# Optimization experiments

Measured on AMD Instinct MI355X. Metric: run time of the kernel, lower is better.

The kernel has to match this reference:

```python
import jax, jax.numpy as jnp
import numpy as np

B, N, C, H = 8, 16384, 256, 128
FG_NPOINT = 4096
SAMPLE_POINT = 1024
MAX_TRANSLATE = jnp.array([3.0, 3.0, 2.0], dtype=jnp.float32)


def _fps(xyz, n_sample):
    # xyz: [N,3] -> indices [n_sample] (D-FPS, seed index 0)
    d0 = jnp.sum((xyz - xyz[0]) ** 2, axis=-1)  # [N]

    def body(dists, _):
        idx = jnp.argmax(dists)
        d = jnp.sum((xyz - xyz[idx]) ** 2, axis=-1)
        return jnp.minimum(dists, d), idx

    _, idxs = jax.lax.scan(body, d0, None, length=n_sample - 1)
    return jnp.concatenate([jnp.zeros((1,), dtype=idxs.dtype), idxs])


def fps_batch(xyz, n_sample):
    return jax.vmap(lambda p: _fps(p, n_sample))(xyz)  # [B, n_sample]


def gather_pts(xyz, idx):
    # xyz [B,N,3], idx [B,S] -> [B,S,3]
    return jnp.take_along_axis(xyz, idx[..., None], axis=1)


def gather_feat(feat, idx):
    # feat [B,C,N], idx [B,S] -> [B,C,S]
    return jnp.take_along_axis(feat, idx[:, None, :], axis=2)


def setup_inputs() -> dict:
    key = jax.random.key(0)
    ks = jax.random.split(key, 6)
    return {
        "xyz": jax.random.normal(ks[0], (B, N, 3), jnp.float32) * 10.0,
        "features": jax.random.normal(ks[1], (B, C, N), jnp.float32),
        "seg_w1": jax.random.normal(ks[2], (H, C), jnp.float32) * 0.05,
        "seg_scale1": jnp.ones((H,), jnp.float32),
        "seg_bias1": jnp.zeros((H,), jnp.float32),
        "seg_w2": jax.random.normal(ks[3], (1, H), jnp.float32) * 0.05,
        "seg_b2": jnp.zeros((1,), jnp.float32),
        "vote_w1": jax.random.normal(ks[4], (H, C), jnp.float32) * 0.05,
        "vote_scale1": jnp.ones((H,), jnp.float32),
        "vote_bias1": jnp.zeros((H,), jnp.float32),
        "reg_w": jax.random.normal(ks[5], (3, H), jnp.float32) * 0.05,
        "reg_b": jnp.zeros((3,), jnp.float32),
    }


def reference(xyz, features, seg_w1, seg_scale1, seg_bias1, seg_w2, seg_b2,
              vote_w1, vote_scale1, vote_bias1, reg_w, reg_b):
    # ---- seg branch: 1x1 conv + BN(eval affine) + ReLU, then 1x1 conv to num_class
    h = jax.nn.relu(jnp.einsum('oc,bcn->bon', seg_w1, features)
                    * seg_scale1[None, :, None] + seg_bias1[None, :, None])
    seg = jnp.einsum('oc,bon->bcn'.replace('c', 'k'), seg_w2, h)  # [B,1,N]
    seg = seg + seg_b2[None, :, None]
    seg_score = jax.nn.sigmoid(jnp.max(seg, axis=1))  # [B,N] (max over class dim)

    # ---- top-k foreground selection
    _, fg_idx = jax.lax.top_k(seg_score, FG_NPOINT)  # [B,M]
    fg_xyz = gather_pts(xyz, fg_idx)                  # [B,M,3]
    fg_feat = gather_feat(features, fg_idx)           # [B,C,M]

    # ---- vote/offset layer (3DSSD-style): MLP -> clamped offset
    vh = jax.nn.relu(jnp.einsum('oc,bcm->bom', vote_w1, fg_feat)
                     * vote_scale1[None, :, None] + vote_bias1[None, :, None])  # [B,H,M]
    reg = jnp.einsum('oh,bhm->bom', reg_w, vh) + reg_b[None, :, None]  # [B,3,M]
    offset = jnp.clip(reg.transpose(0, 2, 1), -MAX_TRANSLATE, MAX_TRANSLATE)  # [B,M,3]
    fg_xyz_ctr = fg_xyz + offset
    fg_feat_ctr = vh

    # ---- original-point FPS sampler + gathers
    ori_idx = fps_batch(fg_xyz, SAMPLE_POINT)
    sampled_ori_xyz = gather_pts(fg_xyz, ori_idx)
    sampled_ori_feat = gather_feat(fg_feat, ori_idx)

    # ---- center-point FPS sampler + gathers
    ctr_idx = fps_batch(fg_xyz_ctr, SAMPLE_POINT)
    sampled_ctr_xyz = gather_pts(fg_xyz_ctr, ctr_idx)
    sampled_ctr_feat = gather_feat(fg_feat_ctr, ctr_idx)
    sampled_ctr_offset = gather_pts(offset, ctr_idx)
    sampled_ctr_origin = gather_pts(fg_xyz, ctr_idx)

    # ---- aggregation concat (USE_ORIGINAL_POINT=True)
    agg_xyz = jnp.concatenate([sampled_ctr_xyz, sampled_ori_xyz], axis=1)       # [B,2S,3]
    agg_feat = jnp.concatenate([sampled_ctr_feat, sampled_ori_feat[:, :H, :]], axis=-1)  # [B,H,2S]

    return (agg_xyz, agg_feat, sampled_ctr_xyz, sampled_ctr_offset,
            sampled_ctr_origin, seg)
```

## Files before the change

### kernel.cpp

```cpp
#include <hip/hip_runtime.h>

#define NB 8
#define NP 16384
#define NC 256
#define NH 128
#define NM 4096
#define NS 1024

typedef float v2f __attribute__((ext_vector_type(2)));

__device__ __forceinline__ unsigned long long make_key(float v, int n) {
  unsigned u = __float_as_uint(v);
  u = (u & 0x80000000u) ? ~u : (u | 0x80000000u);
  unsigned d = ~u;
  return (((unsigned long long)d) << 32) | (unsigned)n;
}

__device__ __forceinline__ float wave_max_dpp(float v) {
#define DPPMAX(ctrl)                                                            \
  v = fmaxf(v, __int_as_float(__builtin_amdgcn_update_dpp(                      \
                 __float_as_int(v), __float_as_int(v), (ctrl), 0xf, 0xf, false)))
  DPPMAX(0xB1);
  DPPMAX(0x4E);
  DPPMAX(0x141);
  DPPMAX(0x140);
  DPPMAX(0x142);
  DPPMAX(0x143);
#undef DPPMAX
  return __int_as_float(__builtin_amdgcn_readlane(__float_as_int(v), 63));
}

__global__ __launch_bounds__(256) void transpose_w_kernel(
    const float* __restrict__ wseg, const float* __restrict__ wvote,
    float* __restrict__ tseg, float* __restrict__ tvote) {
  int i = blockIdx.x * 256 + threadIdx.x;
  int c = i >> 7, o = i & 127;
  tseg[i] = wseg[o * NC + c];
  tvote[i] = wvote[o * NC + c];
}

__global__ __launch_bounds__(256) void seg_kernel(
    const float* __restrict__ features, const float* __restrict__ w1t,
    const float* __restrict__ scale1, const float* __restrict__ bias1,
    const float* __restrict__ w2, const float* __restrict__ b2,
    float* __restrict__ seg_out, unsigned long long* __restrict__ keys) {
  __shared__ float wt[32][128];
  __shared__ float ft[32][128];
  __shared__ float red[16][128];
  __shared__ float Ssh[128];
  __shared__ float w2sh[128];
  int b = blockIdx.y;
  int n0 = blockIdx.x * 128;
  int tid = threadIdx.x;
  int lane = tid & 63;
  int ro = tid >> 4, rc = tid & 15;
  float a0 = w2[lane], a1 = w2[lane + 64];
  float whi = fmaxf(a0, a1), wlo = fminf(a0, a1);
#pragma unroll
  for (int off = 32; off >= 1; off >>= 1) {
    whi = fmaxf(whi, __shfl_xor(whi, off, 64));
    wlo = fminf(wlo, __shfl_xor(wlo, off, 64));
  }
  if (tid < 128) w2sh[tid] = w2[tid];
  const float* fb = features + (size_t)b * NC * NP;
  float acc[8][8] = {};
  for (int kc = 0; kc < NC; kc += 32) {
#pragma unroll
    for (int t = 0; t < 4; ++t) {
      int q = tid + t * 256;
      int kk = q >> 5, c4 = (q & 31) * 4;
      *(float4*)&wt[kk][c4] = *(const float4*)&w1t[(kc + kk) * NH + c4];
    }
#pragma unroll
    for (int t = 0; t < 4; ++t) {
      int q = tid + t * 256;
      int kk = q >> 5, c4 = (q & 31) * 4;
      *(float4*)&ft[kk][c4] = *(const float4*)&fb[(size_t)(kc + kk) * NP + n0 + c4];
    }
    __syncthreads();
#pragma unroll
    for (int kk = 0; kk < 32; ++kk) {
      float wv[8], fv[8];
#pragma unroll
      for (int i = 0; i < 8; ++i) wv[i] = wt[kk][ro * 8 + i];
#pragma unroll
      for (int j = 0; j < 8; ++j) fv[j] = ft[kk][rc * 8 + j];
#pragma unroll
      for (int i = 0; i < 8; ++i)
#pragma unroll
        for (int j = 0; j < 8; ++j) acc[i][j] = fmaf(wv[i], fv[j], acc[i][j]);
    }
    __syncthreads();
  }
  float part[8] = {};
#pragma unroll
  for (int i = 0; i < 8; ++i) {
    int o = ro * 8 + i;
    float sc = scale1[o], bi = bias1[o];
#pragma unroll
    for (int j = 0; j < 8; ++j) {
      float h = fmaxf(fmaf(acc[i][j], sc, bi), 0.0f);
      part[j] += h;
    }
  }
#pragma unroll
  for (int j = 0; j < 8; ++j) red[ro][rc * 8 + j] = part[j];
  __syncthreads();
  float b2v = b2[0];
  if (tid < 128) {
    float S = 0.0f;
#pragma unroll
    for (int r = 0; r < 16; ++r) S += red[r][tid];
    Ssh[tid] = S;
    float m = (S >= 0.0f ? whi * S : wlo * S) + b2v;
    float sig = 1.0f / (1.0f + expf(-m));
    int nn = n0 + tid;
    keys[(size_t)b * NP + nn] = make_key(sig, nn);
  }
  __syncthreads();
#pragma unroll
  for (int t = 0; t < 16; ++t) {
    int q = tid + t * 256;
    int k = q >> 5, n4 = (q & 31) * 4;
    float w2k = w2sh[k];
    const float4 s4 = *(const float4*)&Ssh[n4];
    float4 sv;
    sv.x = fmaf(w2k, s4.x, b2v);
    sv.y = fmaf(w2k, s4.y, b2v);
    sv.z = fmaf(w2k, s4.z, b2v);
    sv.w = fmaf(w2k, s4.w, b2v);
    *(float4*)&seg_out[((size_t)b * 128 + k) * NP + n0 + n4] = sv;
  }
}

__global__ __launch_bounds__(1024) void sort8k_kernel(unsigned long long* __restrict__ keys) {
  __shared__ unsigned long long sk[8192];
  int chunk = blockIdx.x & 1, b = blockIdx.x >> 1;
  bool desc = (chunk == 1);
  unsigned long long* K = keys + (size_t)b * NP + chunk * 8192;
  int tid = threadIdx.x;
  for (int i = tid; i < 8192; i += 1024) sk[i] = K[i];
  __syncthreads();
  for (int k = 2; k <= 8192; k <<= 1) {
    for (int j = k >> 1; j > 0; j >>= 1) {
      for (int i = tid; i < 8192; i += 1024) {
        int ixj = i ^ j;
        if (ixj > i) {
          bool up = (((i & k) == 0) != desc);
          unsigned long long a = sk[i], c = sk[ixj];
          if ((a > c) == up) { sk[i] = c; sk[ixj] = a; }
        }
      }
      __syncthreads();
    }
  }
  for (int i = tid; i < 8192; i += 1024) K[i] = sk[i];
}

__global__ __launch_bounds__(1024) void merge_topk_kernel(
    const unsigned long long* __restrict__ keys, int* __restrict__ fg_idx,
    float* __restrict__ fg_xyz, const float* __restrict__ xyz) {
  __shared__ unsigned long long sk[8192];
  int b = blockIdx.x;
  const unsigned long long* K = keys + (size_t)b * NP;
  int tid = threadIdx.x;
  for (int i = tid; i < 8192; i += 1024) {
    unsigned long long a = K[i], c = K[i + 8192];
    sk[i] = (a < c) ? a : c;
  }
  __syncthreads();
  for (int j = 4096; j > 0; j >>= 1) {
    for (int i = tid; i < 8192; i += 1024) {
      int ixj = i ^ j;
      if (ixj > i) {
        unsigned long long a = sk[i], c = sk[ixj];
        if (a > c) { sk[i] = c; sk[ixj] = a; }
      }
    }
    __syncthreads();
  }
  for (int m = tid; m < NM; m += 1024) {
    unsigned long long key = sk[m];
    int idx = (int)(key & 0xffffffffULL);
    fg_idx[b * NM + m] = idx;
    size_t src = ((size_t)b * NP + idx) * 3;
    size_t dst = ((size_t)b * NM + m) * 3;
    fg_xyz[dst + 0] = xyz[src + 0];
    fg_xyz[dst + 1] = xyz[src + 1];
    fg_xyz[dst + 2] = xyz[src + 2];
  }
}

__global__ __launch_bounds__(256) void vote_kernel(
    const float* __restrict__ features, const int* __restrict__ fg_idx,
    const float* __restrict__ w1t, const float* __restrict__ scale1,
    const float* __restrict__ bias1, const float* __restrict__ rw,
    const float* __restrict__ rb, const float* __restrict__ fg_xyz,
    float* __restrict__ vh, float* __restrict__ offs, float* __restrict__ fg_ctr) {
  __shared__ float wt[32][128];
  __shared__ float ft[32][64];
  __shared__ float hl[128][65];
  __shared__ int idx_l[64];
  int b = blockIdx.y;
  int m0 = blockIdx.x * 64;
  int tid = threadIdx.x;
  int ro = tid >> 4, rc = tid & 15;
  const float* fb = features + (size_t)b * NC * NP;
  if (tid < 64) idx_l[tid] = fg_idx[b * NM + m0 + tid];
  __syncthreads();
  float acc[8][4] = {};
  for (int kc = 0; kc < NC; kc += 32) {
    for (int q = tid; q < 4096; q += 256) {
      int kk = q >> 7, o = q & 127;
      wt[kk][o] = w1t[(kc + kk) * NH + o];
    }
    for (int q = tid; q < 2048; q += 256) {
      int kk = q >> 6, mm = q & 63;
      ft[kk][mm] = fb[(size_t)(kc + kk) * NP + idx_l[mm]];
    }
    __syncthreads();
#pragma unroll
    for (int kk = 0; kk < 32; ++kk) {
      float wv[8], fv[4];
#pragma unroll
      for (int i = 0; i < 8; ++i) wv[i] = wt[kk][ro * 8 + i];
#pragma unroll
      for (int j = 0; j < 4; ++j) fv[j] = ft[kk][rc * 4 + j];
#pragma unroll
      for (int i = 0; i < 8; ++i)
#pragma unroll
        for (int j = 0; j < 4; ++j) acc[i][j] = fmaf(wv[i], fv[j], acc[i][j]);
    }
    __syncthreads();
  }
#pragma unroll
  for (int i = 0; i < 8; ++i) {
    int o = ro * 8 + i;
    float sc = scale1[o], bi = bias1[o];
#pragma unroll
    for (int j = 0; j < 4; ++j) {
      float h = fmaxf(fmaf(acc[i][j], sc, bi), 0.0f);
      hl[o][rc * 4 + j] = h;
      vh[((size_t)b * NH + o) * NM + m0 + rc * 4 + j] = h;
    }
  }
  __syncthreads();
  if (tid < 64) {
    int m = m0 + tid;
    const float MT[3] = {3.0f, 3.0f, 2.0f};
#pragma unroll
    for (int r = 0; r < 3; ++r) {
      float a = 0.0f;
      for (int o = 0; o < NH; ++o) a = fmaf(rw[r * NH + o], hl[o][tid], a);
      a += rb[r];
      a = fminf(fmaxf(a, -MT[r]), MT[r]);
      size_t p = ((size_t)b * NM + m) * 3 + r;
      offs[p] = a;
      fg_ctr[p] = __fadd_rn(fg_xyz[p], a);
    }
  }
}

#define PPT 16
__global__ __launch_bounds__(256) void fps_kernel(
    const float* __restrict__ fg_xyz, const float* __restrict__ fg_ctr,
    int* __restrict__ ori_idx, int* __restrict__ ctr_idx) {
#pragma clang fp contract(off)
  __shared__ float px[NM], py[NM], pz[NM];
  __shared__ __align__(32) unsigned long long wkey[2][4];
  __shared__ int sel_list[NS];
  int set = blockIdx.x & 1, b = blockIdx.x >> 1;
  const float* P = (set == 0 ? fg_xyz : fg_ctr) + (size_t)b * NM * 3;
  int* O = (set == 0 ? ori_idx : ctr_idx) + b * NS;
  int tid = threadIdx.x;
  for (int m = tid; m < NM; m += 256) {
    px[m] = P[m * 3 + 0];
    py[m] = P[m * 3 + 1];
    pz[m] = P[m * 3 + 2];
  }
  __syncthreads();
  v2f x2[8], y2[8], z2[8], d2[8];
  int base_idx = tid * PPT;
#pragma unroll
  for (int j = 0; j < 8; ++j) {
    int m0 = base_idx + 2 * j, m1 = m0 + 1;
    v2f t;
    t.x = px[m0]; t.y = px[m1]; x2[j] = t;
    t.x = py[m0]; t.y = py[m1]; y2[j] = t;
    t.x = pz[m0]; t.y = pz[m1]; z2[j] = t;
    t.x = 3.402823466e38f; t.y = 3.402823466e38f;
    d2[j] = t;
  }
  if (tid == 0) sel_list[0] = 0;
  int lane = tid & 63, wave = tid >> 6;
  float sx = px[0], sy = py[0], sz = pz[0];
  for (int it = 1; it < NS; ++it) {
    v2f sxv, syv, szv;
    sxv.x = sx; sxv.y = sx;
    syv.x = sy; syv.y = sy;
    szv.x = sz; szv.y = sz;
    float bd = -1.0f;
    int bc = base_idx;
#pragma unroll
    for (int j = 0; j < 8; ++j) {
      v2f dx = x2[j] - sxv, dy = y2[j] - syv, dz = z2[j] - szv;
      v2f dd = (dx * dx + dy * dy) + dz * dz;
      v2f nd;
      nd.x = fminf(d2[j].x, dd.x);
      nd.y = fminf(d2[j].y, dd.y);
      d2[j] = nd;
      if (j == 0) {
        bd = nd.x; bc = base_idx;
        bool g = nd.y > bd; bd = g ? nd.y : bd; bc = g ? base_idx + 1 : bc;
      } else {
        bool g0 = nd.x > bd; bd = g0 ? nd.x : bd; bc = g0 ? base_idx + 2 * j : bc;
        bool g1 = nd.y > bd; bd = g1 ? nd.y : bd; bc = g1 ? base_idx + 2 * j + 1 : bc;
      }
    }
    float wm = wave_max_dpp(bd);
    unsigned long long msk = __ballot(bd == wm);
    int wl = __ffsll((long long)msk) - 1;
    if (lane == wl)
      wkey[it & 1][wave] =
          (((unsigned long long)__float_as_uint(bd)) << 32) | (unsigned)(4095 - bc);
    __syncthreads();
    const ulonglong2* wk = (const ulonglong2*)&wkey[it & 1][0];
    ulonglong2 q0 = wk[0], q1 = wk[1];
    unsigned long long m0 = q0.x > q0.y ? q0.x : q0.y;
    unsigned long long m1 = q1.x > q1.y ? q1.x : q1.y;
    unsigned long long km = m0 > m1 ? m0 : m1;
    int sel = 4095 - (int)(km & 0xffffffffULL);
    if (tid == 0) sel_list[it] = sel;
    sx = px[sel]; sy = py[sel]; sz = pz[sel];
  }
  __syncthreads();
  for (int s2 = tid; s2 < NS; s2 += 256) O[s2] = sel_list[s2];
}

__global__ __launch_bounds__(256) void feat_out_kernel(
    const float* __restrict__ vh, const float* __restrict__ features,
    const int* __restrict__ fg_idx, const int* __restrict__ ori_idx,
    const int* __restrict__ ctr_idx, float* __restrict__ out_feat) {
  int b = blockIdx.z;
  int o = blockIdx.y * 4 + (threadIdx.x >> 6);
  int s = blockIdx.x * 64 + (threadIdx.x & 63);
  float val;
  if (s < NS) {
    int i = ctr_idx[b * NS + s];
    val = vh[((size_t)b * NH + o) * NM + i];
  } else {
    int i = ori_idx[b * NS + (s - NS)];
    int g = fg_idx[b * NM + i];
    val = features[((size_t)b * NC + o) * NP + g];
  }
  out_feat[((size_t)b * NH + o) * (2 * NS) + s] = val;
}

__global__ __launch_bounds__(256) void xyz_out_kernel(
    const float* __restrict__ fg_xyz, const float* __restrict__ fg_ctr,
    const float* __restrict__ offs, const int* __restrict__ ori_idx,
    const int* __restrict__ ctr_idx, float* __restrict__ out_agg,
    float* __restrict__ out_cxyz, float* __restrict__ out_coff,
    float* __restrict__ out_corg) {
  int b = blockIdx.y;
  int s = blockIdx.x * 256 + threadIdx.x;
  if (s < NS) {
    int i = ctr_idx[b * NS + s];
    size_t src = ((size_t)b * NM + i) * 3;
    size_t d_agg = ((size_t)b * 2 * NS + s) * 3;
    size_t d_s = ((size_t)b * NS + s) * 3;
#pragma unroll
    for (int r = 0; r < 3; ++r) {
      float c = fg_ctr[src + r];
      out_agg[d_agg + r] = c;
      out_cxyz[d_s + r] = c;
      out_coff[d_s + r] = offs[src + r];
      out_corg[d_s + r] = fg_xyz[src + r];
    }
  } else {
    int i = ori_idx[b * NS + (s - NS)];
    size_t src = ((size_t)b * NM + i) * 3;
    size_t d_agg = ((size_t)b * 2 * NS + s) * 3;
#pragma unroll
    for (int r = 0; r < 3; ++r) out_agg[d_agg + r] = fg_xyz[src + r];
  }
}

extern "C" void kernel_launch(void* const* d_in, const int* in_sizes, int n_in,
                              void* d_out, int out_size, void* d_ws, size_t ws_size,
                              hipStream_t stream) {
  const float* xyz = (const float*)d_in[0];
  const float* features = (const float*)d_in[1];
  const float* seg_w1 = (const float*)d_in[2];
  const float* seg_scale1 = (const float*)d_in[3];
  const float* seg_bias1 = (const float*)d_in[4];
  const float* seg_w2 = (const float*)d_in[5];
  const float* seg_b2 = (const float*)d_in[6];
  const float* vote_w1 = (const float*)d_in[7];
  const float* vote_scale1 = (const float*)d_in[8];
  const float* vote_bias1 = (const float*)d_in[9];
  const float* reg_w = (const float*)d_in[10];
  const float* reg_b = (const float*)d_in[11];
  float* out = (float*)d_out;

  char* ws = (char*)d_ws;
  unsigned long long* keys = (unsigned long long*)(ws + 0);
  int* fg_idx = (int*)(ws + 1048576);
  float* fg_xyz = (float*)(ws + 1179648);
  float* fg_ctr = (float*)(ws + 1572864);
  float* offs = (float*)(ws + 1966080);
  int* ori_idx = (int*)(ws + 2359296);
  int* ctr_idx = (int*)(ws + 2392064);
  float* vh = (float*)(ws + 2424832);
  float* w1t_s = (float*)(ws + 19202048);
  float* w1t_v = (float*)(ws + 19333120);

  float* out_agg_xyz = out;
  float* out_agg_feat = out + 49152;
  float* out_ctr_xyz = out + 2146304;
  float* out_ctr_off = out + 2170880;
  float* out_ctr_org = out + 2195456;
  float* out_seg = out + 2220032;

  transpose_w_kernel<<<128, 256, 0, stream>>>(seg_w1, vote_w1, w1t_s, w1t_v);
  seg_kernel<<<dim3(NP / 128, NB), 256, 0, stream>>>(
      features, w1t_s, seg_scale1, seg_bias1, seg_w2, seg_b2, out_seg, keys);
  sort8k_kernel<<<2 * NB, 1024, 0, stream>>>(keys);
  merge_topk_kernel<<<NB, 1024, 0, stream>>>(keys, fg_idx, fg_xyz, xyz);
  vote_kernel<<<dim3(NM / 64, NB), 256, 0, stream>>>(
      features, fg_idx, w1t_v, vote_scale1, vote_bias1, reg_w, reg_b, fg_xyz,
      vh, offs, fg_ctr);
  fps_kernel<<<16, 256, 0, stream>>>(fg_xyz, fg_ctr, ori_idx, ctr_idx);
  feat_out_kernel<<<dim3(32, 32, NB), 256, 0, stream>>>(
      vh, features, fg_idx, ori_idx, ctr_idx, out_agg_feat);
  xyz_out_kernel<<<dim3(8, NB), 256, 0, stream>>>(
      fg_xyz, fg_ctr, offs, ori_idx, ctr_idx, out_agg_xyz, out_ctr_xyz,
      out_ctr_off, out_ctr_org);
}
```

Before: 970.0 us.

## Fuse bitonic sort stages into register-level multi-step passes in shared memory

Rewrites the bitonic sort and the merge kernel so that each thread loads 8 (or 4) keys into registers and performs three (or two) compare-exchange stages before writing back. The final strides 4/2/1 are handled entirely within a thread's contiguous 8-element chunk. This cuts the number of __syncthreads barriers and shared-memory round trips per sort. In exchange it needs more registers and more involved index arithmetic, and the index remapping carries some risk of getting the ordering wrong.

```diff
diff --git a/kernel.cpp b/kernel.cpp
--- a/kernel.cpp
+++ b/kernel.cpp
@@ -14,6 +14,11 @@
   u = (u & 0x80000000u) ? ~u : (u | 0x80000000u);
   unsigned d = ~u;
   return (((unsigned long long)d) << 32) | (unsigned)n;
+}
+
+__device__ __forceinline__ void ce64(unsigned long long& a, unsigned long long& c, bool up) {
+  unsigned long long x = a, y = c;
+  if ((x > y) == up) { a = y; c = x; }
 }
 
 __device__ __forceinline__ float wave_max_dpp(float v) {
@@ -142,17 +147,72 @@
   for (int i = tid; i < 8192; i += 1024) sk[i] = K[i];
   __syncthreads();
   for (int k = 2; k <= 8192; k <<= 1) {
-    for (int j = k >> 1; j > 0; j >>= 1) {
-      for (int i = tid; i < 8192; i += 1024) {
-        int ixj = i ^ j;
-        if (ixj > i) {
-          bool up = (((i & k) == 0) != desc);
-          unsigned long long a = sk[i], c = sk[ixj];
-          if ((a > c) == up) { sk[i] = c; sk[ixj] = a; }
+    int j = k >> 1;
+    while (j >= 8) {
+      if (j >= 32) {
+        int ja = j, jb = j >> 1, jc = j >> 2;
+        int x = tid;
+        x = (x & (jc - 1)) | ((x & ~(jc - 1)) << 1);
+        x = (x & (jb - 1)) | ((x & ~(jb - 1)) << 1);
+        x = (x & (ja - 1)) | ((x & ~(ja - 1)) << 1);
+        unsigned long long e[8];
+        e[0] = sk[x];           e[1] = sk[x | jc];
+        e[2] = sk[x | jb];      e[3] = sk[x | jb | jc];
+        e[4] = sk[x | ja];      e[5] = sk[x | ja | jc];
+        e[6] = sk[x | ja | jb]; e[7] = sk[x | ja | jb | jc];
+        bool up = ((x & k) == 0) != desc;
+        ce64(e[0], e[4], up); ce64(e[1], e[5], up); ce64(e[2], e[6], up); ce64(e[3], e[7], up);
+        ce64(e[0], e[2], up); ce64(e[1], e[3], up); ce64(e[4], e[6], up); ce64(e[5], e[7], up);
+        ce64(e[0], e[1], up); ce64(e[2], e[3], up); ce64(e[4], e[5], up); ce64(e[6], e[7], up);
+        sk[x] = e[0];           sk[x | jc] = e[1];
+        sk[x | jb] = e[2];      sk[x | jb | jc] = e[3];
+        sk[x | ja] = e[4];      sk[x | ja | jc] = e[5];
+        sk[x | ja | jb] = e[6]; sk[x | ja | jb | jc] = e[7];
+        j >>= 3;
+      } else if (j >= 16) {
+        int ja = j, jb = j >> 1;
+        for (int g = tid; g < 2048; g += 1024) {
+          int x = g;
+          x = (x & (jb - 1)) | ((x & ~(jb - 1)) << 1);
+          x = (x & (ja - 1)) | ((x & ~(ja - 1)) << 1);
+          unsigned long long e0 = sk[x], e1 = sk[x | jb];
+          unsigned long long e2 = sk[x | ja], e3 = sk[x | ja | jb];
+          bool up = ((x & k) == 0) != desc;
+          ce64(e0, e2, up); ce64(e1, e3, up);
+          ce64(e0, e1, up); ce64(e2, e3, up);
+          sk[x] = e0; sk[x | jb] = e1; sk[x | ja] = e2; sk[x | ja | jb] = e3;
         }
+        j >>= 2;
+      } else {
+        for (int g = tid; g < 4096; g += 1024) {
+          int i = (g & 7) | ((g & ~7) << 1);
+          bool up = ((i & k) == 0) != desc;
+          unsigned long long a = sk[i], c = sk[i | 8];
+          if ((a > c) == up) { sk[i] = c; sk[i | 8] = a; }
+        }
+        j >>= 1;
       }
       __syncthreads();
     }
+    {
+      int base = tid * 8;
+      unsigned long long e[8];
+#pragma unroll
+      for (int t = 0; t < 8; ++t) e[t] = sk[base + t];
+#pragma unroll
+      for (int jj = 4; jj >= 1; jj >>= 1) {
+        if (jj > (k >> 1)) continue;
+#pragma unroll
+        for (int t = 0; t < 8; ++t)
+          if (!(t & jj)) {
+            bool up = (((base + t) & k) == 0) != desc;
+            ce64(e[t], e[t | jj], up);
+          }
+      }
+#pragma unroll
+      for (int t = 0; t < 8; ++t) sk[base + t] = e[t];
+    }
+    __syncthreads();
   }
   for (int i = tid; i < 8192; i += 1024) K[i] = sk[i];
 }
@@ -169,16 +229,62 @@
     sk[i] = (a < c) ? a : c;
   }
   __syncthreads();
-  for (int j = 4096; j > 0; j >>= 1) {
-    for (int i = tid; i < 8192; i += 1024) {
-      int ixj = i ^ j;
-      if (ixj > i) {
-        unsigned long long a = sk[i], c = sk[ixj];
-        if (a > c) { sk[i] = c; sk[ixj] = a; }
+  int j = 4096;
+  while (j >= 8) {
+    if (j >= 32) {
+      int ja = j, jb = j >> 1, jc = j >> 2;
+      int x = tid;
+      x = (x & (jc - 1)) | ((x & ~(jc - 1)) << 1);
+      x = (x & (jb - 1)) | ((x & ~(jb - 1)) << 1);
+      x = (x & (ja - 1)) | ((x & ~(ja - 1)) << 1);
+      unsigned long long e[8];
+      e[0] = sk[x];           e[1] = sk[x | jc];
+      e[2] = sk[x | jb];      e[3] = sk[x | jb | jc];
+      e[4] = sk[x | ja];      e[5] = sk[x | ja | jc];
+      e[6] = sk[x | ja | jb]; e[7] = sk[x | ja | jb | jc];
+      ce64(e[0], e[4], true); ce64(e[1], e[5], true); ce64(e[2], e[6], true); ce64(e[3], e[7], true);
+      ce64(e[0], e[2], true); ce64(e[1], e[3], true); ce64(e[4], e[6], true); ce64(e[5], e[7], true);
+      ce64(e[0], e[1], true); ce64(e[2], e[3], true); ce64(e[4], e[5], true); ce64(e[6], e[7], true);
+      sk[x] = e[0];           sk[x | jc] = e[1];
+      sk[x | jb] = e[2];      sk[x | jb | jc] = e[3];
+      sk[x | ja] = e[4];      sk[x | ja | jc] = e[5];
+      sk[x | ja | jb] = e[6]; sk[x | ja | jb | jc] = e[7];
+      j >>= 3;
+    } else if (j >= 16) {
+      int ja = j, jb = j >> 1;
+      for (int g = tid; g < 2048; g += 1024) {
+        int x = g;
+        x = (x & (jb - 1)) | ((x & ~(jb - 1)) << 1);
+        x = (x & (ja - 1)) | ((x & ~(ja - 1)) << 1);
+        unsigned long long e0 = sk[x], e1 = sk[x | jb];
+        unsigned long long e2 = sk[x | ja], e3 = sk[x | ja | jb];
+        ce64(e0, e2, true); ce64(e1, e3, true);
+        ce64(e0, e1, true); ce64(e2, e3, true);
+        sk[x] = e0; sk[x | jb] = e1; sk[x | ja] = e2; sk[x | ja | jb] = e3;
       }
-    }
-    __syncthreads();
-  }
+      j >>= 2;
+    } else {
+      for (int g = tid; g < 4096; g += 1024) {
+        int i = (g & 7) | ((g & ~7) << 1);
+        unsigned long long a = sk[i], c = sk[i | 8];
+        if (a > c) { sk[i] = c; sk[i | 8] = a; }
+      }
+      j >>= 1;
+    }
+    __syncthreads();
+  }
+  {
+    int base = tid * 8;
+    unsigned long long e[8];
+#pragma unroll
+    for (int t = 0; t < 8; ++t) e[t] = sk[base + t];
+    ce64(e[0], e[4], true); ce64(e[1], e[5], true); ce64(e[2], e[6], true); ce64(e[3], e[7], true);
+    ce64(e[0], e[2], true); ce64(e[1], e[3], true); ce64(e[4], e[6], true); ce64(e[5], e[7], true);
+    ce64(e[0], e[1], true); ce64(e[2], e[3], true); ce64(e[4], e[5], true); ce64(e[6], e[7], true);
+#pragma unroll
+    for (int t = 0; t < 8; ++t) sk[base + t] = e[t];
+  }
+  __syncthreads();
   for (int m = tid; m < NM; m += 1024) {
     unsigned long long key = sk[m];
     int idx = (int)(key & 0xffffffffULL);
```

Result: faster. 897.7 us (-7.5%).
